# Performance work log

Measured on AMD Instinct MI355X. Metric: run time of the kernel, lower is better.

The kernel has to match this reference:

```python
import jax, jax.numpy as jnp
import numpy as np

EPS = 1e-8

def render_point_cloud(xyz, data, h, w):
    """Soft z-buffer splatting: nearest-pixel scatter with inverse-depth weights.
    xyz: (bs, p, 3) NDC coords; data: (bs, c, p). Returns (bs,c,h,w), (bs,1,h,w), (bs,p) bool."""
    bs, c, p = data.shape
    x = (xyz[..., 0] + 1.0) * 0.5 * (w - 1)   # NDC -> pixel coords
    y = (xyz[..., 1] + 1.0) * 0.5 * (h - 1)
    z = xyz[..., 2]
    viz = (x > -0.5) & (x < w - 0.5) & (y > -0.5) & (y < h - 0.5) & (z > 0)  # (bs,p)
    xi = jnp.clip(jnp.round(x), 0, w - 1).astype(jnp.int32)
    yi = jnp.clip(jnp.round(y), 0, h - 1).astype(jnp.int32)
    # inverse-depth confidence weight; invisible points contribute nothing
    wgt = jnp.where(viz, 1.0 / jnp.maximum(z, EPS), 0.0)  # (bs,p)
    pix = yi * w + xi                                      # (bs,p)
    seg = (jnp.arange(bs, dtype=jnp.int32)[:, None] * (h * w) + pix).reshape(-1)  # (bs*p,)
    feat = (data * wgt[:, None, :]).transpose(0, 2, 1).reshape(bs * p, c)
    acc = jax.ops.segment_sum(feat, seg, num_segments=bs * h * w)          # (bs*h*w, c)
    conf = jax.ops.segment_sum(wgt.reshape(-1), seg, num_segments=bs * h * w)
    acc = acc.reshape(bs, h, w, c).transpose(0, 3, 1, 2)   # (bs,c,h,w)
    conf = conf.reshape(bs, 1, h, w)
    out = acc / jnp.maximum(conf, EPS)                     # weight-normalized splat
    return out, conf, viz


def setup_inputs() -> dict:
    key = jax.random.key(0)
    k1, k2, k3 = jax.random.split(key, 3)
    bs, p, c, h, w = 4, 262144, 32, 512, 512
    xy = jax.random.uniform(k1, (bs, p, 2), dtype=jnp.float32, minval=-1.05, maxval=1.05)
    z = jax.random.uniform(k2, (bs, p, 1), dtype=jnp.float32, minval=0.5, maxval=5.0)
    xyz = jnp.concatenate([xy, z], axis=-1)               # (bs,p,3)
    data = jax.random.normal(k3, (bs, c, p), dtype=jnp.float32)
    return {"xyz": xyz, "data": data, "h": h, "w": w}


def reference(xyz, data, h, w):
    assert xyz.shape[1] == data.shape[2]
    out, conf, viz = render_point_cloud(xyz, data, h, w)
    return out, conf, viz
```

## Files before the change

### kernel.cpp

```cpp
#include <hip/hip_runtime.h>

#define BS 4
#define P  262144
#define C  32
#define H  512
#define W  512
#define HW (H * W)
#define NEPS 1e-8f


#define TP 256
#define SPAD (TP + 4)

__device__ inline void pk_add_bf16(unsigned short* p, unsigned int v)
{
    asm volatile("global_atomic_pk_add_bf16 %0, %1, off"
                 :: "v"(p), "v"(v) : "memory");
}

__device__ inline unsigned int pack_bf16_rne(float a, float b)
{
    unsigned int ua = __builtin_bit_cast(unsigned int, a);
    unsigned int ub = __builtin_bit_cast(unsigned int, b);
    ua += 0x7FFFu + ((ua >> 16) & 1u);
    ub += 0x7FFFu + ((ub >> 16) & 1u);
    return (ua >> 16) | (ub & 0xFFFF0000u);
}
__device__ inline float bf16_lo(unsigned int w) { return __builtin_bit_cast(float, w << 16); }
__device__ inline float bf16_hi(unsigned int w) { return __builtin_bit_cast(float, w & 0xFFFF0000u); }

__global__ __launch_bounds__(256) void splat_scatter_t(
    const float* __restrict__ xyz, const float* __restrict__ data,
    unsigned short* __restrict__ acc, float* __restrict__ conf,
    float* __restrict__ viz)
{
    __shared__ __align__(16) unsigned int s_pk[C / 2][SPAD];
    __shared__ float s_xyz[TP * 3];
    __shared__ float s_wgt[TP];
    __shared__ int   s_pix[TP];

    const int t    = threadIdx.x;
    const int base = blockIdx.x * TP;
    const int b    = base >> 18;
    const int j0   = base & (P - 1);

    if (t < 192) {
        float4 v = ((const float4*)(xyz + (size_t)base * 3))[t];
        s_xyz[t * 4 + 0] = v.x;
        s_xyz[t * 4 + 1] = v.y;
        s_xyz[t * 4 + 2] = v.z;
        s_xyz[t * 4 + 3] = v.w;
    }

    const float4* dsrc = (const float4*)(data + (size_t)b * C * P + j0);
    #pragma unroll
    for (int i = 0; i < 4; ++i) {
        int e = i * 256 + t;
        int c = e >> 6;
        int q = e & 63;
        float4 va = dsrc[(size_t)(2 * c + 0) * (P / 4) + q];
        float4 vb = dsrc[(size_t)(2 * c + 1) * (P / 4) + q];
        uint4 r;
        r.x = pack_bf16_rne(va.x, vb.x);
        r.y = pack_bf16_rne(va.y, vb.y);
        r.z = pack_bf16_rne(va.z, vb.z);
        r.w = pack_bf16_rne(va.w, vb.w);
        *(uint4*)&s_pk[c][4 * q] = r;
    }
    __syncthreads();

    {
        float x = s_xyz[3 * t + 0];
        float y = s_xyz[3 * t + 1];
        float z = s_xyz[3 * t + 2];
        float px = (x + 1.0f) * 0.5f * (float)(W - 1);
        float py = (y + 1.0f) * 0.5f * (float)(H - 1);
        bool v = (px > -0.5f) && (px < (float)W - 0.5f) &&
                 (py > -0.5f) && (py < (float)H - 0.5f) && (z > 0.0f);
        viz[base + t] = v ? 1.0f : 0.0f;
        int pix = -1;
        float wg = 0.0f;
        if (v) {
            int xi = (int)fminf(fmaxf(rintf(px), 0.0f), (float)(W - 1));
            int yi = (int)fminf(fmaxf(rintf(py), 0.0f), (float)(H - 1));
            pix = yi * W + xi;
            wg  = 1.0f / fmaxf(z, NEPS);
            unsafeAtomicAdd(&conf[b * HW + pix], wg);
        }
        s_pix[t] = pix;
        s_wgt[t] = wg;
    }
    __syncthreads();

    const int g = t >> 4;
    const int d = t & 15;
    #pragma unroll
    for (int k = 0; k < TP / 16; ++k) {
        int jj  = k * 16 + g;
        int pix = s_pix[jj];
        if (pix >= 0) {
            float wg = s_wgt[jj];
            unsigned int pk = s_pk[d][jj];
            pk_add_bf16(acc + (((size_t)b << 18) + pix) * C + 2 * d,
                        pack_bf16_rne(bf16_lo(pk) * wg, bf16_hi(pk) * wg));
        }
    }
}

__global__ __launch_bounds__(256) void splat_transpose_norm(
    const unsigned short* __restrict__ acc, const float* __restrict__ conf,
    float* __restrict__ out)
{
    __shared__ float s_t[64][C + 1];
    __shared__ float s_inv[64];

    const int t    = threadIdx.x;
    const int blk  = blockIdx.x;
    const int b    = blk >> 12;
    const int pix0 = (blk & ((HW / 64) - 1)) * 64;

    if (t < 64)
        s_inv[t] = 1.0f / fmaxf(conf[(size_t)b * HW + pix0 + t], NEPS);

    const uint4* src = (const uint4*)(acc + ((size_t)b * HW + pix0) * C);
    {
        uint4 v = src[t];
        int po  = t >> 2;
        int ch0 = (t & 3) * 8;
        unsigned int ws[4] = {v.x, v.y, v.z, v.w};
        #pragma unroll
        for (int w = 0; w < 4; ++w) {
            s_t[po][ch0 + 2 * w + 0] = bf16_lo(ws[w]);
            s_t[po][ch0 + 2 * w + 1] = bf16_hi(ws[w]);
        }
    }
    __syncthreads();

    #pragma unroll
    for (int i = 0; i < 8; ++i) {
        int e  = i * 256 + t;
        int ch = e >> 6;
        int po = e & 63;
        out[((size_t)b * C + ch) * HW + pix0 + po] = s_t[po][ch] * s_inv[po];
    }
}


__global__ __launch_bounds__(256) void splat_scatter_fb(
    const float* __restrict__ xyz, const float* __restrict__ data,
    float* __restrict__ acc, float* __restrict__ conf, float* __restrict__ viz)
{
    int idx = blockIdx.x * 256 + threadIdx.x;
    if (idx >= BS * P) return;
    int b = idx >> 18;
    int j = idx & (P - 1);
    float x = xyz[3 * idx + 0], y = xyz[3 * idx + 1], z = xyz[3 * idx + 2];
    float px = (x + 1.0f) * 0.5f * (float)(W - 1);
    float py = (y + 1.0f) * 0.5f * (float)(H - 1);
    bool v = (px > -0.5f) && (px < (float)W - 0.5f) &&
             (py > -0.5f) && (py < (float)H - 0.5f) && (z > 0.0f);
    viz[idx] = v ? 1.0f : 0.0f;
    if (!v) return;
    int xi = (int)fminf(fmaxf(rintf(px), 0.0f), (float)(W - 1));
    int yi = (int)fminf(fmaxf(rintf(py), 0.0f), (float)(H - 1));
    float wg = 1.0f / fmaxf(z, NEPS);
    int pix = yi * W + xi;
    unsafeAtomicAdd(&conf[b * HW + pix], wg);
    const float* db = data + (size_t)b * C * P + j;
    float*       ab = acc  + (size_t)b * C * HW + pix;
    #pragma unroll
    for (int ch = 0; ch < C; ++ch)
        unsafeAtomicAdd(ab + (size_t)ch * HW, db[(size_t)ch * P] * wg);
}

__global__ __launch_bounds__(256) void splat_norm_fb(
    float* __restrict__ out, const float* __restrict__ conf)
{
    int idx = blockIdx.x * 256 + threadIdx.x;
    if (idx >= BS * HW) return;
    int b   = idx >> 18;
    int pix = idx & (HW - 1);
    float inv = 1.0f / fmaxf(conf[idx], NEPS);
    float* ob = out + (size_t)b * C * HW + pix;
    #pragma unroll
    for (int ch = 0; ch < C; ++ch)
        ob[(size_t)ch * HW] *= inv;
}

extern "C" void kernel_launch(void* const* d_in, const int* in_sizes, int n_in,
                              void* d_out, int out_size, void* d_ws, size_t ws_size,
                              hipStream_t stream)
{
    const float* xyz  = (const float*)d_in[0];
    const float* data = (const float*)d_in[1];

    float* out  = (float*)d_out;
    float* conf = out  + (size_t)BS * C * HW;
    float* viz  = conf + (size_t)BS * HW;

    const size_t acc_bytes = (size_t)BS * HW * C * sizeof(unsigned short);

    if (ws_size >= acc_bytes) {
        unsigned short* acc = (unsigned short*)d_ws;
        (void)hipMemsetAsync(acc, 0, acc_bytes, stream);
        (void)hipMemsetAsync(conf, 0, (size_t)BS * HW * sizeof(float), stream);
        splat_scatter_t<<<BS * P / TP, 256, 0, stream>>>(xyz, data, acc, conf, viz);
        splat_transpose_norm<<<BS * HW / 64, 256, 0, stream>>>(acc, conf, out);
    } else {
        (void)hipMemsetAsync(d_out, 0, (size_t)(BS * C * HW + BS * HW) * sizeof(float), stream);
        splat_scatter_fb<<<(BS * P + 255) / 256, 256, 0, stream>>>(xyz, data, out, conf, viz);
        splat_norm_fb<<<(BS * HW + 255) / 256, 256, 0, stream>>>(out, conf);
    }
}
```

Measured before the change: 151.3 us.

## Interleave conf into 128-byte per-pixel accumulator records and shrink point tile

Each pixel's accumulator becomes a 128-byte record: 32 bf16 channel sums plus an fp32 confidence at dword 16. The conf atomic therefore lands in the same cache line as the channel atomics, and the separate conf memset goes away. The transpose kernel reads conf from the record and writes it to the output. The scatter kernel now uses 64-point tiles with fp32 features in shared memory instead of bf16 packing before the atomic. The cost is that the workspace memset doubles to about 134 MB, and if the workspace is too small the slow fallback path runs.

```diff
diff --git a/kernel.cpp b/kernel.cpp
--- a/kernel.cpp
+++ b/kernel.cpp
@@ -9,8 +9,7 @@
 #define NEPS 1e-8f
 
 
-#define TP 256
-#define SPAD (TP + 4)
+#define TP 64
 
 __device__ inline void pk_add_bf16(unsigned short* p, unsigned int v)
 {
@@ -31,10 +30,9 @@
 
 __global__ __launch_bounds__(256) void splat_scatter_t(
     const float* __restrict__ xyz, const float* __restrict__ data,
-    unsigned short* __restrict__ acc, float* __restrict__ conf,
-    float* __restrict__ viz)
-{
-    __shared__ __align__(16) unsigned int s_pk[C / 2][SPAD];
+    unsigned int* __restrict__ acc2, float* __restrict__ viz)
+{
+    __shared__ float s_feat[C][TP + 1];
     __shared__ float s_xyz[TP * 3];
     __shared__ float s_wgt[TP];
     __shared__ int   s_pix[TP];
@@ -44,32 +42,28 @@
     const int b    = base >> 18;
     const int j0   = base & (P - 1);
 
-    if (t < 192) {
+    const float4* dsrc = (const float4*)(data + (size_t)b * C * P + j0);
+    #pragma unroll
+    for (int i = 0; i < 2; ++i) {
+        int f4 = i * 256 + t;
+        int ch = f4 >> 4;
+        int q  = f4 & 15;
+        float4 v = dsrc[(size_t)ch * (P / 4) + q];
+        s_feat[ch][q * 4 + 0] = v.x;
+        s_feat[ch][q * 4 + 1] = v.y;
+        s_feat[ch][q * 4 + 2] = v.z;
+        s_feat[ch][q * 4 + 3] = v.w;
+    }
+    if (t < 48) {
         float4 v = ((const float4*)(xyz + (size_t)base * 3))[t];
         s_xyz[t * 4 + 0] = v.x;
         s_xyz[t * 4 + 1] = v.y;
         s_xyz[t * 4 + 2] = v.z;
         s_xyz[t * 4 + 3] = v.w;
     }
-
-    const float4* dsrc = (const float4*)(data + (size_t)b * C * P + j0);
-    #pragma unroll
-    for (int i = 0; i < 4; ++i) {
-        int e = i * 256 + t;
-        int c = e >> 6;
-        int q = e & 63;
-        float4 va = dsrc[(size_t)(2 * c + 0) * (P / 4) + q];
-        float4 vb = dsrc[(size_t)(2 * c + 1) * (P / 4) + q];
-        uint4 r;
-        r.x = pack_bf16_rne(va.x, vb.x);
-        r.y = pack_bf16_rne(va.y, vb.y);
-        r.z = pack_bf16_rne(va.z, vb.z);
-        r.w = pack_bf16_rne(va.w, vb.w);
-        *(uint4*)&s_pk[c][4 * q] = r;
-    }
     __syncthreads();
 
-    {
+    if (t < TP) {
         float x = s_xyz[3 * t + 0];
         float y = s_xyz[3 * t + 1];
         float z = s_xyz[3 * t + 2];
@@ -85,7 +79,6 @@
             int yi = (int)fminf(fmaxf(rintf(py), 0.0f), (float)(H - 1));
             pix = yi * W + xi;
             wg  = 1.0f / fmaxf(z, NEPS);
-            unsafeAtomicAdd(&conf[b * HW + pix], wg);
         }
         s_pix[t] = pix;
         s_wgt[t] = wg;
@@ -100,16 +93,19 @@
         int pix = s_pix[jj];
         if (pix >= 0) {
             float wg = s_wgt[jj];
-            unsigned int pk = s_pk[d][jj];
-            pk_add_bf16(acc + (((size_t)b << 18) + pix) * C + 2 * d,
-                        pack_bf16_rne(bf16_lo(pk) * wg, bf16_hi(pk) * wg));
+            size_t rec_dw = (((size_t)b << 18) + pix) * 32;
+            pk_add_bf16((unsigned short*)acc2 + rec_dw * 2 + 2 * d,
+                        pack_bf16_rne(s_feat[2 * d + 0][jj] * wg,
+                                      s_feat[2 * d + 1][jj] * wg));
+            if (d == 0)
+                unsafeAtomicAdd((float*)acc2 + rec_dw + 16, wg);
         }
     }
 }
 
 __global__ __launch_bounds__(256) void splat_transpose_norm(
-    const unsigned short* __restrict__ acc, const float* __restrict__ conf,
-    float* __restrict__ out)
+    const unsigned int* __restrict__ acc2,
+    float* __restrict__ out, float* __restrict__ conf_out)
 {
     __shared__ float s_t[64][C + 1];
     __shared__ float s_inv[64];
@@ -119,14 +115,19 @@
     const int b    = blk >> 12;
     const int pix0 = (blk & ((HW / 64) - 1)) * 64;
 
-    if (t < 64)
-        s_inv[t] = 1.0f / fmaxf(conf[(size_t)b * HW + pix0 + t], NEPS);
-
-    const uint4* src = (const uint4*)(acc + ((size_t)b * HW + pix0) * C);
+    const unsigned int* rb = acc2 + ((size_t)b * HW + pix0) * 32;
+
+    if (t < 64) {
+        float cf = __builtin_bit_cast(float, rb[(size_t)t * 32 + 16]);
+        conf_out[(size_t)b * HW + pix0 + t] = cf;
+        s_inv[t] = 1.0f / fmaxf(cf, NEPS);
+    }
+
     {
-        uint4 v = src[t];
-        int po  = t >> 2;
-        int ch0 = (t & 3) * 8;
+        int po = t >> 2;
+        int q  = t & 3;
+        uint4 v = *(const uint4*)(rb + (size_t)po * 32 + q * 4);
+        int ch0 = q * 8;
         unsigned int ws[4] = {v.x, v.y, v.z, v.w};
         #pragma unroll
         for (int w = 0; w < 4; ++w) {
@@ -198,14 +199,13 @@
     float* conf = out  + (size_t)BS * C * HW;
     float* viz  = conf + (size_t)BS * HW;
 
-    const size_t acc_bytes = (size_t)BS * HW * C * sizeof(unsigned short);
-
-    if (ws_size >= acc_bytes) {
-        unsigned short* acc = (unsigned short*)d_ws;
-        (void)hipMemsetAsync(acc, 0, acc_bytes, stream);
-        (void)hipMemsetAsync(conf, 0, (size_t)BS * HW * sizeof(float), stream);
-        splat_scatter_t<<<BS * P / TP, 256, 0, stream>>>(xyz, data, acc, conf, viz);
-        splat_transpose_norm<<<BS * HW / 64, 256, 0, stream>>>(acc, conf, out);
+    const size_t acc2_bytes = (size_t)BS * HW * 128;
+
+    if (ws_size >= acc2_bytes) {
+        unsigned int* acc2 = (unsigned int*)d_ws;
+        (void)hipMemsetAsync(acc2, 0, acc2_bytes, stream);
+        splat_scatter_t<<<BS * P / TP, 256, 0, stream>>>(xyz, data, acc2, viz);
+        splat_transpose_norm<<<BS * HW / 64, 256, 0, stream>>>(acc2, out, conf);
     } else {
         (void)hipMemsetAsync(d_out, 0, (size_t)(BS * C * HW + BS * HW) * sizeof(float), stream);
         splat_scatter_fb<<<(BS * P + 255) / 256, 256, 0, stream>>>(xyz, data, out, conf, viz);
```

Measured after the change: 174.7 us. +15.4%, slower.
